# Kernel optimization log

Measured on AMD Instinct MI355X. Metric: run time of the kernel, lower is better.

Reference implementation:

```python
import jax, jax.numpy as jnp
import numpy as np

N = 65536          # total nodes across batch
C = 256            # in channels
COUT = 256         # out channels
B = 8              # batch size (graphs)
EMB = 512          # emb channels
N_EDGE_TYPE = 7
N_NODE_TYPE = 7
AVG_DEGREE = 7
E = N * AVG_DEGREE
GROUP = 32         # min(32, channels)
EPS = 1e-5


def setup_inputs() -> dict:
    key = jax.random.key(0)
    ks = jax.random.split(key, 10)
    # GraphConv init: uniform xavier-like with fan scaled by avg_degree
    std = (2.0 / float(AVG_DEGREE * C + AVG_DEGREE * COUT)) ** 0.5
    a = (3.0 ** 0.5) * std
    return {
        "x": jax.random.normal(ks[0], (N, C), jnp.float32),
        "emb": jax.random.normal(ks[1], (B, EMB), jnp.float32),
        "batch_id": jnp.sort(jax.random.randint(ks[2], (N,), 0, B, jnp.int32)),
        "edge_index": jax.random.randint(ks[3], (2, E), 0, N, jnp.int32),
        "edge_type": jax.random.randint(ks[4], (E,), 0, N_EDGE_TYPE, jnp.int32),
        "node_type": jax.random.randint(ks[5], (N,), 0, N_NODE_TYPE, jnp.int32),
        "gn1_w": jnp.ones((1, C), jnp.float32),
        "gn1_b": jnp.zeros((1, C), jnp.float32),
        "conv1_w": jax.random.uniform(ks[6], (N_EDGE_TYPE * (C + N_NODE_TYPE), COUT), jnp.float32, -a, a),
        "emb_w": jax.random.normal(ks[7], (EMB, COUT), jnp.float32) * 0.02,
        "emb_b": jnp.zeros((COUT,), jnp.float32),
        "gn2_w": jnp.ones((1, COUT), jnp.float32),
        "gn2_b": jnp.zeros((1, COUT), jnp.float32),
        "conv2_w": jax.random.uniform(ks[8], (N_EDGE_TYPE * (COUT + N_NODE_TYPE), COUT), jnp.float32, -a, a),
    }


def _adjust_for_group(t, cpg):
    # sum stats within each group of cpg channels, broadcast back: [B, C]
    if cpg > 1:
        Bsz, Cn = t.shape
        g = Cn // cpg
        t = t.reshape(Bsz, g, cpg).sum(-1, keepdims=True)
        t = jnp.broadcast_to(t, (Bsz, g, cpg)).reshape(Bsz, Cn)
    return t


def dual_octree_group_norm(data, batch_id, w, b):
    # data: [N, C]; per-graph group norm via segment sums
    Cn = data.shape[1]
    cpg = Cn // GROUP
    ones = jnp.ones((data.shape[0], 1), data.dtype)
    count = jax.ops.segment_sum(ones, batch_id, num_segments=B) * cpg   # [B,1]
    inv_count = 1.0 / (count + EPS)
    mean = jax.ops.segment_sum(data, batch_id, num_segments=B) * inv_count
    mean = _adjust_for_group(mean, cpg)
    out = data - mean[batch_id]
    var = jax.ops.segment_sum(out * out, batch_id, num_segments=B) * inv_count
    var = _adjust_for_group(var, cpg)
    inv_std = 1.0 / jnp.sqrt(var + EPS)
    out = out * inv_std[batch_id]
    return out * w + b


def graph_conv(x, weights, edge_index, edge_type, node_type):
    # concat one-hot node type channels
    one_hot = jax.nn.one_hot(node_type, N_NODE_TYPE, dtype=x.dtype)
    xa = jnp.concatenate([x, one_hot], axis=1)          # [N, C+T]
    row, col = edge_index[0], edge_index[1]
    index = row * N_EDGE_TYPE + edge_type               # [E]
    col_data = jax.ops.segment_sum(xa[col], index, num_segments=xa.shape[0] * N_EDGE_TYPE)
    return col_data.reshape(xa.shape[0], -1) @ weights  # [N, COUT]


def reference(x, emb, batch_id, edge_index, edge_type, node_type,
              gn1_w, gn1_b, conv1_w, emb_w, emb_b, gn2_w, gn2_b, conv2_w):
    h = dual_octree_group_norm(x, batch_id, gn1_w, gn1_b)
    h = jax.nn.silu(h)
    h = graph_conv(h, conv1_w, edge_index, edge_type, node_type)
    emb_out = jax.nn.silu(emb) @ emb_w + emb_b          # [B, COUT]
    h = h + emb_out[batch_id]                           # per-batch add (loop in torch)
    h = dual_octree_group_norm(h, batch_id, gn2_w, gn2_b)
    h = jax.nn.silu(h)                                  # dropout p=0 -> identity
    h = graph_conv(h, conv2_w, edge_index, edge_type, node_type)
    return x + h                                        # skip is Identity (Cout==C)
```

## Files before the change

kernel.cpp:

```cpp
#include <hip/hip_runtime.h>
#include <math.h>

#define N_NODES 65536
#define B_GR    8
#define EMB_N   512
#define E_EDGES 458752
#define NSEG    458752
#define TSTRIDE 288
#define GK      2016
#define EPS     1e-5f

typedef unsigned short u16;
typedef unsigned int   u32;
typedef __bf16 bf16x8 __attribute__((ext_vector_type(8)));
typedef float  f32x4  __attribute__((ext_vector_type(4)));
typedef u16    u16x8  __attribute__((ext_vector_type(8)));

__device__ __forceinline__ float bf2f(u16 u) {
    u32 x = ((u32)u) << 16; float f; __builtin_memcpy(&f, &x, 4); return f;
}
__device__ __forceinline__ u16 f2bf(float f) {
    u32 x; __builtin_memcpy(&x, &f, 4);
    u32 r = x + 0x7fffu + ((x >> 16) & 1u);
    return (u16)(r >> 16);
}

__global__ __launch_bounds__(256) void zero_kernel(int* __restrict__ hist,
                                                   float* __restrict__ S, float* __restrict__ Q) {
    int i = blockIdx.x * 256 + threadIdx.x;
    if (i < NSEG) hist[i] = 0;
    if (i < 2048) { S[i] = 0.f; Q[i] = 0.f; }
}
__global__ __launch_bounds__(256) void zero_sq_kernel(float* __restrict__ S, float* __restrict__ Q) {
    int i = blockIdx.x * 256 + threadIdx.x;
    if (i < 2048) { S[i] = 0.f; Q[i] = 0.f; }
}

__global__ __launch_bounds__(256) void prep_kernel(
    const float* __restrict__ w1, const float* __restrict__ w2,
    u16* __restrict__ Wt1, u16* __restrict__ Wt2,
    const float* __restrict__ emb, const float* __restrict__ embw,
    const float* __restrict__ embb, float* __restrict__ embout)
{
    int bid = blockIdx.x, tid = threadIdx.x;
    if (bid < 4032) {
        const float* Win = (bid < 2016) ? w1 : w2;
        u16* Wt = (bid < 2016) ? Wt1 : Wt2;
        int idx = (bid % 2016) * 256 + tid;
        int n = idx / GK;
        int k = idx - n * GK;
        int t = k / TSTRIDE;
        int c = k - t * TSTRIDE;
        u16 v = (c < 263) ? f2bf(Win[(size_t)(t * 263 + c) * 256 + n]) : (u16)0;
        Wt[idx] = v;
    } else {
        __shared__ float semb[B_GR * EMB_N];
        for (int i = tid; i < B_GR * EMB_N; i += 256) {
            float e = emb[i];
            semb[i] = e / (1.f + expf(-e));
        }
        __syncthreads();
        float acc[8];
        float bb = embb[tid];
#pragma unroll
        for (int b = 0; b < 8; b++) acc[b] = bb;
        for (int k = 0; k < EMB_N; k++) {
            float wv = embw[k * 256 + tid];
#pragma unroll
            for (int b = 0; b < 8; b++) acc[b] += semb[b * EMB_N + k] * wv;
        }
#pragma unroll
        for (int b = 0; b < 8; b++) embout[b * 256 + tid] = acc[b];
    }
}

__global__ __launch_bounds__(256) void stats_kernel(const float* __restrict__ xin,
                                                    const int* __restrict__ batch_id,
                                                    float* __restrict__ S, float* __restrict__ Q) {
    int c = threadIdx.x;
    int n0 = blockIdx.x * 64;
    float s = 0.f, q = 0.f;
    int bcur = batch_id[n0];
    for (int r = 0; r < 64; r++) {
        int n = n0 + r;
        int b = batch_id[n];
        if (b != bcur) {
            atomicAdd(&S[bcur * 256 + c], s);
            atomicAdd(&Q[bcur * 256 + c], q);
            s = 0.f; q = 0.f; bcur = b;
        }
        float v = xin[(size_t)n * 256 + c];
        s += v;
        q = fmaf(v, v, q);
    }
    atomicAdd(&S[bcur * 256 + c], s);
    atomicAdd(&Q[bcur * 256 + c], q);
}

__global__ __launch_bounds__(256) void finalize_kernel(const int* __restrict__ batch_id,
                                                       const float* __restrict__ S, const float* __restrict__ Q,
                                                       float* __restrict__ gmean, float* __restrict__ gistd) {
    __shared__ int scnt[8];
    int tid = threadIdx.x;
    if (tid < 8) scnt[tid] = 0;
    __syncthreads();
    int c0=0,c1=0,c2=0,c3=0,c4=0,c5=0,c6=0,c7=0;
    for (int i = tid; i < N_NODES; i += 256) {
        int b = batch_id[i];
        c0 += (b==0); c1 += (b==1); c2 += (b==2); c3 += (b==3);
        c4 += (b==4); c5 += (b==5); c6 += (b==6); c7 += (b==7);
    }
    atomicAdd(&scnt[0], c0); atomicAdd(&scnt[1], c1); atomicAdd(&scnt[2], c2); atomicAdd(&scnt[3], c3);
    atomicAdd(&scnt[4], c4); atomicAdd(&scnt[5], c5); atomicAdd(&scnt[6], c6); atomicAdd(&scnt[7], c7);
    __syncthreads();
    int b = tid >> 5, g = tid & 31;
    float Sg = 0.f, Qg = 0.f;
#pragma unroll
    for (int k = 0; k < 8; k++) {
        Sg += S[b * 256 + g * 8 + k];
        Qg += Q[b * 256 + g * 8 + k];
    }
    float cnt8 = (float)scnt[b] * 8.f;
    float D = cnt8 + EPS;
    float m = Sg / D;
    float var = (Qg - 2.f * m * Sg + cnt8 * m * m) / D;
    float istd = rsqrtf(var + EPS);
    gmean[tid] = m;
    gistd[tid] = istd;
}

__global__ __launch_bounds__(256) void norm_silu_kernel(const float* __restrict__ xin,
                                                        const int* __restrict__ batch_id,
                                                        const float* __restrict__ gmean, const float* __restrict__ gistd,
                                                        const float* __restrict__ w, const float* __restrict__ bias,
                                                        u16* __restrict__ yout) {
    int tid = threadIdx.x;
    int n = blockIdx.x * 8 + (tid >> 5);
    int g = tid & 31;
    int c0 = g * 8;
    int b = batch_id[n];
    float m = gmean[b * 32 + g], is = gistd[b * 32 + g];
    u16x8 o;
#pragma unroll
    for (int k = 0; k < 8; k++) {
        float v = (xin[(size_t)n * 256 + c0 + k] - m) * is;
        v = v * w[c0 + k] + bias[c0 + k];
        v = v / (1.f + expf(-v));
        o[k] = f2bf(v);
    }
    *(u16x8*)&yout[(size_t)n * 256 + c0] = o;
}

__global__ __launch_bounds__(256) void hist_kernel(const int* __restrict__ ei, const int* __restrict__ et,
                                                   int* __restrict__ hist) {
    int e = blockIdx.x * 256 + threadIdx.x;
    if (e >= E_EDGES) return;
    int s = ei[e] * 7 + et[e];
    atomicAdd(&hist[s], 1);
}

__global__ __launch_bounds__(512) void scan1_kernel(const int* __restrict__ hist, int* __restrict__ partials) {
    __shared__ int sd[512];
    int i = blockIdx.x * 512 + threadIdx.x;
    sd[threadIdx.x] = hist[i];
    __syncthreads();
    for (int off = 256; off > 0; off >>= 1) {
        if (threadIdx.x < off) sd[threadIdx.x] += sd[threadIdx.x + off];
        __syncthreads();
    }
    if (threadIdx.x == 0) partials[blockIdx.x] = sd[0];
}

__global__ __launch_bounds__(1024) void scan2_kernel(int* __restrict__ partials) {
    __shared__ int sd[1024];
    int t = threadIdx.x;
    int v = (t < 896) ? partials[t] : 0;
    sd[t] = v;
    __syncthreads();
    for (int off = 1; off < 1024; off <<= 1) {
        int u = (t >= off) ? sd[t - off] : 0;
        __syncthreads();
        sd[t] += u;
        __syncthreads();
    }
    if (t < 896) partials[t] = sd[t] - v;
}

__global__ __launch_bounds__(512) void scan3_kernel(int* __restrict__ hist_offs, const int* __restrict__ partials,
                                                    int* __restrict__ cursor) {
    __shared__ int sd[512];
    int t = threadIdx.x;
    int i = blockIdx.x * 512 + t;
    int c = hist_offs[i];
    sd[t] = c;
    __syncthreads();
    for (int off = 1; off < 512; off <<= 1) {
        int u = (t >= off) ? sd[t - off] : 0;
        __syncthreads();
        sd[t] += u;
        __syncthreads();
    }
    int o = partials[blockIdx.x] + sd[t] - c;
    hist_offs[i] = o;
    cursor[i] = o;
}

__global__ __launch_bounds__(256) void fill_kernel(const int* __restrict__ ei, const int* __restrict__ et,
                                                   int* __restrict__ cursor, int* __restrict__ elist) {
    int e = blockIdx.x * 256 + threadIdx.x;
    if (e >= E_EDGES) return;
    int s = ei[e] * 7 + et[e];
    int p = atomicAdd(&cursor[s], 1);
    if (p >= 0 && p < E_EDGES) elist[p] = ei[E_EDGES + e];
}

__global__ __launch_bounds__(512, 2) void gemm_fused_kernel(
    const u16* __restrict__ y, const u16* __restrict__ Bt,
    const int* __restrict__ offs, const int* __restrict__ cursor,
    const int* __restrict__ elist, const int* __restrict__ node_type,
    const int* __restrict__ batch_id, const float* __restrict__ embout,
    const float* __restrict__ xres, float* __restrict__ out, int mode)
{
    __shared__ __align__(16) u16 As[128 * 32];
    __shared__ __align__(16) u16 Bs[256 * 32];
    int tid = threadIdx.x;
    int lane = tid & 63, w = tid >> 6;
    int wm = w >> 2, wn = w & 3;
    int lm = lane & 15, lq = lane >> 4;
    int m0 = blockIdx.x * 128;

    f32x4 acc[4][4];
    f32x4 zz = {0.f, 0.f, 0.f, 0.f};
#pragma unroll
    for (int i = 0; i < 4; i++)
#pragma unroll
        for (int j = 0; j < 4; j++) acc[i][j] = zz;

    int ar = tid >> 2, aq = tid & 3;

    for (int kk = 0; kk < GK; kk += 32) {
        int t = kk / TSTRIDE;
        int c0 = kk - t * TSTRIDE;
        __syncthreads();
#pragma unroll
        for (int i2 = 0; i2 < 2; i2++) {
            int q = tid + i2 * 512;
            int row = q >> 2, k8 = q & 3;
            *(u16x8*)&Bs[q * 8] = *(const u16x8*)&Bt[(size_t)row * GK + kk + k8 * 8];
        }
        int s = (m0 + ar) * 7 + t;
        int start = offs[s], end = cursor[s];
        float a8[8] = {0.f,0.f,0.f,0.f,0.f,0.f,0.f,0.f};
        if (c0 < 256) {
            int cbase = c0 + aq * 8;
            for (int e = start; e < end; e++) {
                int col = elist[e];
                u16x8 v = *(const u16x8*)&y[(size_t)col * 256 + cbase];
#pragma unroll
                for (int j = 0; j < 8; j++) a8[j] += bf2f(v[j]);
            }
        } else if (aq == 0) {
            for (int e = start; e < end; e++) {
                int nt = node_type[elist[e]];
#pragma unroll
                for (int j = 0; j < 7; j++) a8[j] += (nt == j) ? 1.f : 0.f;
            }
        }
        u16x8 o;
#pragma unroll
        for (int j = 0; j < 8; j++) o[j] = f2bf(a8[j]);
        *(u16x8*)&As[ar * 32 + aq * 8] = o;
        __syncthreads();
        bf16x8 a[4], b[4];
#pragma unroll
        for (int i = 0; i < 4; i++) a[i] = *(const bf16x8*)&As[(wm * 64 + i * 16 + lm) * 32 + lq * 8];
#pragma unroll
        for (int j = 0; j < 4; j++) b[j] = *(const bf16x8*)&Bs[(wn * 64 + j * 16 + lm) * 32 + lq * 8];
#pragma unroll
        for (int i = 0; i < 4; i++)
#pragma unroll
            for (int j = 0; j < 4; j++)
                acc[i][j] = __builtin_amdgcn_mfma_f32_16x16x32_bf16(a[i], b[j], acc[i][j], 0, 0, 0);
    }

#pragma unroll
    for (int i = 0; i < 4; i++) {
#pragma unroll
        for (int r = 0; r < 4; r++) {
            size_t m = (size_t)m0 + wm * 64 + i * 16 + lq * 4 + r;
            float addv[4];
            if (mode == 0) {
                int b = batch_id[m];
#pragma unroll
                for (int j = 0; j < 4; j++) addv[j] = embout[b * 256 + wn * 64 + j * 16 + lm];
            } else {
#pragma unroll
                for (int j = 0; j < 4; j++) addv[j] = xres[m * 256 + wn * 64 + j * 16 + lm];
            }
#pragma unroll
            for (int j = 0; j < 4; j++) {
                int n = wn * 64 + j * 16 + lm;
                out[m * 256 + n] = acc[i][j][r] + addv[j];
            }
        }
    }
}

extern "C" void kernel_launch(void* const* d_in, const int* in_sizes, int n_in,
                              void* d_out, int out_size, void* d_ws, size_t ws_size,
                              hipStream_t stream) {
    const float* x    = (const float*)d_in[0];
    const float* emb  = (const float*)d_in[1];
    const int* bid    = (const int*)d_in[2];
    const int* ei     = (const int*)d_in[3];
    const int* et     = (const int*)d_in[4];
    const int* ntp    = (const int*)d_in[5];
    const float* gn1w = (const float*)d_in[6];
    const float* gn1b = (const float*)d_in[7];
    const float* w1   = (const float*)d_in[8];
    const float* embw = (const float*)d_in[9];
    const float* embb = (const float*)d_in[10];
    const float* gn2w = (const float*)d_in[11];
    const float* gn2b = (const float*)d_in[12];
    const float* w2   = (const float*)d_in[13];
    float* out = (float*)d_out;

    char* p = (char*)d_ws;
    size_t off = 0;
    auto nxt = [&](size_t bytes) -> void* {
        void* r = p + off;
        off += (bytes + 255) & ~(size_t)255;
        return r;
    };
    u16*   y       = (u16*)nxt((size_t)N_NODES * 256 * 2);
    u16*   Wt1     = (u16*)nxt((size_t)256 * GK * 2);
    u16*   Wt2     = (u16*)nxt((size_t)256 * GK * 2);
    float* embout  = (float*)nxt(8 * 256 * 4);
    float* S       = (float*)nxt(2048 * 4);
    float* Q       = (float*)nxt(2048 * 4);
    float* gmean   = (float*)nxt(256 * 4);
    float* gistd   = (float*)nxt(256 * 4);
    int*   offs    = (int*)nxt((size_t)NSEG * 4);
    int*   cursor  = (int*)nxt((size_t)NSEG * 4);
    int*   parts   = (int*)nxt(1024 * 4);
    int*   elist   = (int*)nxt((size_t)E_EDGES * 4);
    float* h2      = out;
    (void)ws_size; (void)in_sizes; (void)n_in; (void)out_size;

    zero_kernel<<<1792, 256, 0, stream>>>(offs, S, Q);
    prep_kernel<<<4033, 256, 0, stream>>>(w1, w2, Wt1, Wt2, emb, embw, embb, embout);
    stats_kernel<<<1024, 256, 0, stream>>>(x, bid, S, Q);
    finalize_kernel<<<1, 256, 0, stream>>>(bid, S, Q, gmean, gistd);
    norm_silu_kernel<<<8192, 256, 0, stream>>>(x, bid, gmean, gistd, gn1w, gn1b, y);
    hist_kernel<<<1792, 256, 0, stream>>>(ei, et, offs);
    scan1_kernel<<<896, 512, 0, stream>>>(offs, parts);
    scan2_kernel<<<1, 1024, 0, stream>>>(parts);
    scan3_kernel<<<896, 512, 0, stream>>>(offs, parts, cursor);
    fill_kernel<<<1792, 256, 0, stream>>>(ei, et, cursor, elist);
    gemm_fused_kernel<<<512, 512, 0, stream>>>(y, Wt1, offs, cursor, elist, ntp, bid, embout, x, h2, 0);
    zero_sq_kernel<<<8, 256, 0, stream>>>(S, Q);
    stats_kernel<<<1024, 256, 0, stream>>>(h2, bid, S, Q);
    finalize_kernel<<<1, 256, 0, stream>>>(bid, S, Q, gmean, gistd);
    norm_silu_kernel<<<8192, 256, 0, stream>>>(h2, bid, gmean, gistd, gn2w, gn2b, y);
    gemm_fused_kernel<<<512, 512, 0, stream>>>(y, Wt2, offs, cursor, elist, ntp, bid, embout, x, out, 1);
}
```

Measured before the change: 878.4 us.

## Restructure fused gather-GEMM into software-pipelined 64-row tiles with swizzled LDS

The fused gather+GEMM kernel now uses 64-row tiles with 256 threads and 1024 blocks. It loops over edge types, loading a segment's first four edge columns once and reusing them across all nine K chunks. Gather and weight loads for the next chunk are issued from registers before the current chunk's MFMAs, overlapping memory latency with compute. LDS tiles get an XOR swizzle to cut bank conflicts. In exchange, per-thread register pressure rises and the B tile is reloaded per 64 rows instead of per 128.

```diff
diff --git a/kernel.cpp b/kernel.cpp
--- a/kernel.cpp
+++ b/kernel.cpp
@@ -24,6 +24,8 @@
     u32 r = x + 0x7fffu + ((x >> 16) & 1u);
     return (u16)(r >> 16);
 }
+
+#define SW(row, k8) ((k8) ^ (((row) >> 1) & 3))
 
 __global__ __launch_bounds__(256) void zero_kernel(int* __restrict__ hist,
                                                    float* __restrict__ S, float* __restrict__ Q) {
@@ -214,20 +216,21 @@
     if (p >= 0 && p < E_EDGES) elist[p] = ei[E_EDGES + e];
 }
 
-__global__ __launch_bounds__(512, 2) void gemm_fused_kernel(
+__global__ __launch_bounds__(256) void gemm_fused_kernel(
     const u16* __restrict__ y, const u16* __restrict__ Bt,
     const int* __restrict__ offs, const int* __restrict__ cursor,
     const int* __restrict__ elist, const int* __restrict__ node_type,
     const int* __restrict__ batch_id, const float* __restrict__ embout,
     const float* __restrict__ xres, float* __restrict__ out, int mode)
 {
-    __shared__ __align__(16) u16 As[128 * 32];
+    __shared__ __align__(16) u16 As[64 * 32];
     __shared__ __align__(16) u16 Bs[256 * 32];
     int tid = threadIdx.x;
-    int lane = tid & 63, w = tid >> 6;
-    int wm = w >> 2, wn = w & 3;
+    int lane = tid & 63;
+    int wn = tid >> 6;
     int lm = lane & 15, lq = lane >> 4;
-    int m0 = blockIdx.x * 128;
+    int m0 = blockIdx.x * 64;
+    int ar = tid >> 2, aq = tid & 3;
 
     f32x4 acc[4][4];
     f32x4 zz = {0.f, 0.f, 0.f, 0.f};
@@ -236,58 +239,133 @@
 #pragma unroll
         for (int j = 0; j < 4; j++) acc[i][j] = zz;
 
-    int ar = tid >> 2, aq = tid & 3;
-
-    for (int kk = 0; kk < GK; kk += 32) {
-        int t = kk / TSTRIDE;
-        int c0 = kk - t * TSTRIDE;
-        __syncthreads();
-#pragma unroll
-        for (int i2 = 0; i2 < 2; i2++) {
-            int q = tid + i2 * 512;
-            int row = q >> 2, k8 = q & 3;
-            *(u16x8*)&Bs[q * 8] = *(const u16x8*)&Bt[(size_t)row * GK + kk + k8 * 8];
-        }
+    const u16* btp = Bt + (size_t)ar * GK + aq * 8;
+
+    float a8[8];
+    u16x8 breg[4];
+
+    for (int t = 0; t < 7; t++) {
         int s = (m0 + ar) * 7 + t;
-        int start = offs[s], end = cursor[s];
-        float a8[8] = {0.f,0.f,0.f,0.f,0.f,0.f,0.f,0.f};
-        if (c0 < 256) {
-            int cbase = c0 + aq * 8;
-            for (int e = start; e < end; e++) {
-                int col = elist[e];
-                u16x8 v = *(const u16x8*)&y[(size_t)col * 256 + cbase];
-#pragma unroll
-                for (int j = 0; j < 8; j++) a8[j] += bf2f(v[j]);
-            }
-        } else if (aq == 0) {
-            for (int e = start; e < end; e++) {
-                int nt = node_type[elist[e]];
-#pragma unroll
-                for (int j = 0; j < 7; j++) a8[j] += (nt == j) ? 1.f : 0.f;
-            }
-        }
-        u16x8 o;
-#pragma unroll
-        for (int j = 0; j < 8; j++) o[j] = f2bf(a8[j]);
-        *(u16x8*)&As[ar * 32 + aq * 8] = o;
-        __syncthreads();
-        bf16x8 a[4], b[4];
-#pragma unroll
-        for (int i = 0; i < 4; i++) a[i] = *(const bf16x8*)&As[(wm * 64 + i * 16 + lm) * 32 + lq * 8];
-#pragma unroll
-        for (int j = 0; j < 4; j++) b[j] = *(const bf16x8*)&Bs[(wn * 64 + j * 16 + lm) * 32 + lq * 8];
-#pragma unroll
-        for (int i = 0; i < 4; i++)
-#pragma unroll
-            for (int j = 0; j < 4; j++)
-                acc[i][j] = __builtin_amdgcn_mfma_f32_16x16x32_bf16(a[i], b[j], acc[i][j], 0, 0, 0);
+        int st = offs[s], en = cursor[s];
+        int cnt = en - st;
+        int col[4];
+#pragma unroll
+        for (int u = 0; u < 4; u++) col[u] = (cnt > u) ? elist[st + u] : -1;
+
+#pragma unroll
+        for (int j = 0; j < 8; j++) a8[j] = 0.f;
+        {
+            int cb = aq * 8;
+#pragma unroll
+            for (int u = 0; u < 4; u++)
+                if (col[u] >= 0) {
+                    u16x8 v = *(const u16x8*)&y[(size_t)col[u] * 256 + cb];
+#pragma unroll
+                    for (int j = 0; j < 8; j++) a8[j] += bf2f(v[j]);
+                }
+            if (cnt > 4)
+                for (int e = st + 4; e < en; e++) {
+                    u16x8 v = *(const u16x8*)&y[(size_t)elist[e] * 256 + cb];
+#pragma unroll
+                    for (int j = 0; j < 8; j++) a8[j] += bf2f(v[j]);
+                }
+        }
+        {
+            int kb = t * TSTRIDE;
+#pragma unroll
+            for (int i2 = 0; i2 < 4; i2++) breg[i2] = *(const u16x8*)&btp[(size_t)i2 * 64 * GK + kb];
+        }
+
+#pragma unroll
+        for (int c9 = 0; c9 < 9; c9++) {
+            __syncthreads();
+            u16x8 o;
+#pragma unroll
+            for (int j = 0; j < 8; j++) o[j] = f2bf(a8[j]);
+            *(u16x8*)&As[ar * 32 + SW(ar, aq) * 8] = o;
+#pragma unroll
+            for (int i2 = 0; i2 < 4; i2++) {
+                int row = ar + i2 * 64;
+                *(u16x8*)&Bs[row * 32 + SW(row, aq) * 8] = breg[i2];
+            }
+            __syncthreads();
+            bf16x8 a[4], b[4];
+#pragma unroll
+            for (int i = 0; i < 4; i++) {
+                int ra = i * 16 + lm;
+                a[i] = *(const bf16x8*)&As[ra * 32 + SW(ra, lq) * 8];
+            }
+#pragma unroll
+            for (int j = 0; j < 4; j++) {
+                int rb = wn * 64 + j * 16 + lm;
+                b[j] = *(const bf16x8*)&Bs[rb * 32 + SW(rb, lq) * 8];
+            }
+            u16x8 gv[4];
+            int nt4[4];
+#pragma unroll
+            for (int j = 0; j < 8; j++) a8[j] = 0.f;
+            if (c9 < 7) {
+                int cb = (c9 + 1) * 32 + aq * 8;
+#pragma unroll
+                for (int u = 0; u < 4; u++)
+                    if (col[u] >= 0) gv[u] = *(const u16x8*)&y[(size_t)col[u] * 256 + cb];
+                int kb = t * TSTRIDE + (c9 + 1) * 32;
+#pragma unroll
+                for (int i2 = 0; i2 < 4; i2++) breg[i2] = *(const u16x8*)&btp[(size_t)i2 * 64 * GK + kb];
+            } else if (c9 == 7) {
+                if (aq == 0) {
+#pragma unroll
+                    for (int u = 0; u < 4; u++)
+                        if (col[u] >= 0) nt4[u] = node_type[col[u]];
+                }
+                int kb = t * TSTRIDE + 8 * 32;
+#pragma unroll
+                for (int i2 = 0; i2 < 4; i2++) breg[i2] = *(const u16x8*)&btp[(size_t)i2 * 64 * GK + kb];
+            }
+#pragma unroll
+            for (int i = 0; i < 4; i++)
+#pragma unroll
+                for (int j = 0; j < 4; j++)
+                    acc[i][j] = __builtin_amdgcn_mfma_f32_16x16x32_bf16(a[i], b[j], acc[i][j], 0, 0, 0);
+            if (c9 < 7) {
+#pragma unroll
+                for (int u = 0; u < 4; u++)
+                    if (col[u] >= 0) {
+#pragma unroll
+                        for (int j = 0; j < 8; j++) a8[j] += bf2f(gv[u][j]);
+                    }
+                if (cnt > 4) {
+                    int cb = (c9 + 1) * 32 + aq * 8;
+                    for (int e = st + 4; e < en; e++) {
+                        u16x8 v = *(const u16x8*)&y[(size_t)elist[e] * 256 + cb];
+#pragma unroll
+                        for (int j = 0; j < 8; j++) a8[j] += bf2f(v[j]);
+                    }
+                }
+            } else if (c9 == 7) {
+                if (aq == 0) {
+#pragma unroll
+                    for (int u = 0; u < 4; u++)
+                        if (col[u] >= 0) {
+#pragma unroll
+                            for (int j = 0; j < 7; j++) a8[j] += (nt4[u] == j) ? 1.f : 0.f;
+                        }
+                    if (cnt > 4)
+                        for (int e = st + 4; e < en; e++) {
+                            int nt = node_type[elist[e]];
+#pragma unroll
+                            for (int j = 0; j < 7; j++) a8[j] += (nt == j) ? 1.f : 0.f;
+                        }
+                }
+            }
+        }
     }
 
 #pragma unroll
     for (int i = 0; i < 4; i++) {
 #pragma unroll
         for (int r = 0; r < 4; r++) {
-            size_t m = (size_t)m0 + wm * 64 + i * 16 + lq * 4 + r;
+            size_t m = (size_t)m0 + i * 16 + lq * 4 + r;
             float addv[4];
             if (mode == 0) {
                 int b = batch_id[m];
@@ -357,10 +435,10 @@
     scan2_kernel<<<1, 1024, 0, stream>>>(parts);
     scan3_kernel<<<896, 512, 0, stream>>>(offs, parts, cursor);
     fill_kernel<<<1792, 256, 0, stream>>>(ei, et, cursor, elist);
-    gemm_fused_kernel<<<512, 512, 0, stream>>>(y, Wt1, offs, cursor, elist, ntp, bid, embout, x, h2, 0);
+    gemm_fused_kernel<<<1024, 256, 0, stream>>>(y, Wt1, offs, cursor, elist, ntp, bid, embout, x, h2, 0);
     zero_sq_kernel<<<8, 256, 0, stream>>>(S, Q);
     stats_kernel<<<1024, 256, 0, stream>>>(h2, bid, S, Q);
     finalize_kernel<<<1, 256, 0, stream>>>(bid, S, Q, gmean, gistd);
     norm_silu_kernel<<<8192, 256, 0, stream>>>(h2, bid, gmean, gistd, gn2w, gn2b, y);
-    gemm_fused_kernel<<<512, 512, 0, stream>>>(y, Wt2, offs, cursor, elist, ntp, bid, embout, x, out, 1);
-}
+    gemm_fused_kernel<<<1024, 256, 0, stream>>>(y, Wt2, offs, cursor, elist, ntp, bid, embout, x, out, 1);
+}
```

After: 804.1 us. 8.5% less time.
